# Optimization experiments

Measured on AMD Instinct MI355X. Metric: run time of the kernel, lower is better.

Reference implementation:

```python
import jax, jax.numpy as jnp
import numpy as np

B, N, M, K = 8, 9225, 4096, 32
D = 2          # coordinate dim
HID = 64       # MLP hidden
DOUT = 16      # MLP output / f_y channels


def setup_inputs() -> dict:
    key = jax.random.key(0)
    ks = jax.random.split(key, 10)
    y = jax.random.uniform(ks[0], (B, N, D), dtype=jnp.float32)
    x = jax.random.uniform(ks[1], (B, M, D), dtype=jnp.float32)
    f_y = jax.random.uniform(ks[2], (B, N, DOUT), dtype=jnp.float32)
    weights = jax.random.uniform(ks[3], (B, N), dtype=jnp.float32)
    neighbors_index = jax.random.randint(ks[4], (B, M, K), 0, N, dtype=jnp.int64)
    drop = jax.random.uniform(ks[5], (B, M, K)) < 0.1
    neighbors_index = jnp.where(drop, jnp.int64(-1), neighbors_index)
    # LinearChannelMLP params: 4 -> 64 -> 16, gelu between
    W1 = jax.random.normal(ks[6], (2 * D, HID), dtype=jnp.float32) * (1.0 / np.sqrt(2 * D))
    b1 = jnp.zeros((HID,), dtype=jnp.float32)
    W2 = jax.random.normal(ks[7], (HID, DOUT), dtype=jnp.float32) * (1.0 / np.sqrt(HID))
    b2 = jnp.zeros((DOUT,), dtype=jnp.float32)
    return {"y": y, "x": x, "f_y": f_y, "weights": weights,
            "W1": W1, "b1": b1, "W2": W2, "b2": b2,
            "neighbors_index": neighbors_index}


def _batched_gather(table, idx):
    # table: [B, N, ...], idx: [B, M, K] -> [B, M, K, ...]
    return jax.vmap(lambda t, i: t[i])(table, idx)


def reference(y, x, f_y, weights, W1, b1, W2, b2, neighbors_index):
    idx = jnp.where(neighbors_index == -1, 0, neighbors_index)      # [B,M,K]
    valid = (neighbors_index != -1).astype(y.dtype)[..., None]      # [B,M,K,1]

    rep_y = _batched_gather(y, idx)                                 # [B,M,K,D]
    in_f = _batched_gather(f_y, idx)                                # [B,M,K,DOUT]
    self_x = jnp.broadcast_to(x[:, :, None, :], rep_y.shape)        # [B,M,K,D]

    agg = jnp.concatenate([rep_y, self_x], axis=-1)                 # [B,M,K,2D]
    h = jax.nn.gelu(agg @ W1 + b1, approximate=False)               # [B,M,K,HID]
    kval = h @ W2 + b2                                              # [B,M,K,DOUT]

    kval = kval * in_f                                              # linear transform: k(x,y)*f(y)
    w_nbr = _batched_gather(weights, idx)[..., None]                # [B,M,K,1]
    kval = kval * w_nbr * valid
    return kval.sum(axis=2)                                         # [B,M,DOUT]
```

## Files before the change

### kernel.cpp

```cpp
#include <hip/hip_runtime.h>
#include <hip/hip_bf16.h>
#include <math.h>

#define B_    8
#define N_    9225
#define M_    4096
#define K_    32
#define HID_  64
#define DOUT_ 16
#define RPW   4

typedef __attribute__((ext_vector_type(8))) short short8;
typedef __attribute__((ext_vector_type(4))) float floatx4;
typedef __attribute__((ext_vector_type(2))) float f32x2;

static __device__ __forceinline__ short f2bf(float f) {
    __hip_bfloat16 h = __float2bfloat16(f);
    return __builtin_bit_cast(short, h);
}
static __device__ __forceinline__ f32x2 splat2(float v) { return (f32x2){v, v}; }

static __device__ __forceinline__ float row16_sum(float v) {
    int t;
    t = __builtin_amdgcn_update_dpp(0, __builtin_bit_cast(int, v), 0x111, 0xF, 0xF, true);
    v += __builtin_bit_cast(float, t);
    t = __builtin_amdgcn_update_dpp(0, __builtin_bit_cast(int, v), 0x112, 0xF, 0xF, true);
    v += __builtin_bit_cast(float, t);
    t = __builtin_amdgcn_update_dpp(0, __builtin_bit_cast(int, v), 0x114, 0xF, 0xF, true);
    v += __builtin_bit_cast(float, t);
    t = __builtin_amdgcn_update_dpp(0, __builtin_bit_cast(int, v), 0x118, 0xF, 0xF, true);
    v += __builtin_bit_cast(float, t);
    return v;
}

__global__ __launch_bounds__(256) void it_kernel(
    const float* __restrict__ y,
    const float* __restrict__ x,
    const float* __restrict__ f_y,
    const float* __restrict__ weights,
    const float* __restrict__ W1,
    const float* __restrict__ b1,
    const float* __restrict__ W2,
    const float* __restrict__ b2,
    const int*   __restrict__ nbr,
    float*       __restrict__ out)
{
    const int tid  = threadIdx.x;
    const int lane = tid & 63;
    const int q    = lane >> 4;
    const int nlo  = lane & 15;
    const int wave = blockIdx.x * 4 + (tid >> 6);

    f32x2 w1r[2][4][4];
    f32x2 b1r[2][4];
    #pragma unroll
    for (int ch = 0; ch < 2; ++ch) {
        #pragma unroll
        for (int i = 0; i < 4; ++i) {
            const floatx4 a0 = *(const floatx4*)(W1 + i*64 + ch*32 + q*8);
            const floatx4 a1 = *(const floatx4*)(W1 + i*64 + ch*32 + q*8 + 4);
            w1r[ch][i][0] = (f32x2){a0[0], a0[1]};
            w1r[ch][i][1] = (f32x2){a0[2], a0[3]};
            w1r[ch][i][2] = (f32x2){a1[0], a1[1]};
            w1r[ch][i][3] = (f32x2){a1[2], a1[3]};
        }
        const floatx4 c0 = *(const floatx4*)(b1 + ch*32 + q*8);
        const floatx4 c1 = *(const floatx4*)(b1 + ch*32 + q*8 + 4);
        b1r[ch][0] = (f32x2){c0[0], c0[1]};
        b1r[ch][1] = (f32x2){c0[2], c0[3]};
        b1r[ch][2] = (f32x2){c1[0], c1[1]};
        b1r[ch][3] = (f32x2){c1[2], c1[3]};
    }

    short8 w2f[2];
    #pragma unroll
    for (int ch = 0; ch < 2; ++ch)
        #pragma unroll
        for (int jj = 0; jj < 8; ++jj)
            w2f[ch][jj] = f2bf(W2[(ch*32 + q*8 + jj) * DOUT_ + nlo]);

    const floatx4 b2v = *(const floatx4*)(b2 + q*4);

    for (int it = 0; it < RPW; ++it) {
        const int row = wave * RPW + it;
        const int b   = row >> 12;
        const long bbase = (long)b * N_;
        const float2 xv = *(const float2*)(x + (size_t)row * 2);

        float  s[2]; float2 yv[2]; floatx4 fv[2];
        #pragma unroll
        for (int h = 0; h < 2; ++h) {
            const int  raw   = nbr[(size_t)row * K_ + h*16 + nlo];
            const bool valid = raw >= 0;
            const long bn    = bbase + (valid ? raw : 0);
            yv[h] = *(const float2*)(y + bn * 2);
            s[h]  = valid ? weights[bn] : 0.0f;
            fv[h] = *(const floatx4*)(f_y + bn * 16 + q*4);
        }

        float partial[4] = {0.f, 0.f, 0.f, 0.f};
        #pragma unroll
        for (int h = 0; h < 2; ++h) {
            short8 hf[2];
            #pragma unroll
            for (int ch = 0; ch < 2; ++ch) {
                #pragma unroll
                for (int p = 0; p < 4; ++p) {
                    f32x2 hin = b1r[ch][p];
                    hin = __builtin_elementwise_fma(splat2(yv[h].x), w1r[ch][0][p], hin);
                    hin = __builtin_elementwise_fma(splat2(yv[h].y), w1r[ch][1][p], hin);
                    hin = __builtin_elementwise_fma(splat2(xv.x),    w1r[ch][2][p], hin);
                    hin = __builtin_elementwise_fma(splat2(xv.y),    w1r[ch][3][p], hin);
                    const f32x2 hsq = hin * hin;
                    const f32x2 tt  = __builtin_elementwise_fma(hsq, splat2(0.07135481f),
                                                                splat2(1.59576912f));
                    const f32x2 z   = hin * tt;
                    const float e0  = __expf(z[0]);
                    const float e1  = __expf(z[1]);
                    const f32x2 r   = { __builtin_amdgcn_rcpf(1.0f + e0),
                                        __builtin_amdgcn_rcpf(1.0f + e1) };
                    const f32x2 g   = __builtin_elementwise_fma(-hin, r, hin);
                    hf[ch][2*p]     = f2bf(g[0]);
                    hf[ch][2*p + 1] = f2bf(g[1]);
                }
            }
            floatx4 acc = {0.f, 0.f, 0.f, 0.f};
            acc = __builtin_amdgcn_mfma_f32_16x16x32_bf16(w2f[0], hf[0], acc, 0, 0, 0);
            acc = __builtin_amdgcn_mfma_f32_16x16x32_bf16(w2f[1], hf[1], acc, 0, 0, 0);
            #pragma unroll
            for (int r4 = 0; r4 < 4; ++r4)
                partial[r4] = fmaf(acc[r4] + b2v[r4], fv[h][r4] * s[h], partial[r4]);
        }

        #pragma unroll
        for (int r4 = 0; r4 < 4; ++r4)
            partial[r4] = row16_sum(partial[r4]);

        if (nlo == 15) {
            floatx4 o = {partial[0], partial[1], partial[2], partial[3]};
            *(floatx4*)(out + (size_t)row * DOUT_ + q*4) = o;
        }
    }
}

extern "C" void kernel_launch(void* const* d_in, const int* in_sizes, int n_in,
                              void* d_out, int out_size, void* d_ws, size_t ws_size,
                              hipStream_t stream) {
    const float* y   = (const float*)d_in[0];
    const float* x   = (const float*)d_in[1];
    const float* f_y = (const float*)d_in[2];
    const float* w   = (const float*)d_in[3];
    const float* W1  = (const float*)d_in[4];
    const float* b1  = (const float*)d_in[5];
    const float* W2  = (const float*)d_in[6];
    const float* b2  = (const float*)d_in[7];
    const int*   nbr = (const int*)d_in[8];
    float* out = (float*)d_out;

    dim3 grid(B_ * M_ / (4 * RPW)), block(256);
    hipLaunchKernelGGL(it_kernel, grid, block, 0, stream,
                       y, x, f_y, w, W1, b1, W2, b2, nbr, out);
}
```

Baseline: 109.1 us.

## Prefetch neighbor gathers for all rows and replace exp-based GELU with rational tanh

Halves rows per wave and issues every row's gathers before any compute, so memory latency overlaps across rows and the grid has twice as many waves. It also swaps the exp plus reciprocal tanh-form GELU for a clamped Padé rational approximation of tanh that needs no exp. This holds more registers per wave, doubles weight-setup overhead per row, and adds approximation error on top of the existing tanh-vs-erf difference.

```diff
diff --git a/kernel.cpp b/kernel.cpp
--- a/kernel.cpp
+++ b/kernel.cpp
@@ -8,7 +8,7 @@
 #define K_    32
 #define HID_  64
 #define DOUT_ 16
-#define RPW   4
+#define RPW   2
 
 typedef __attribute__((ext_vector_type(8))) short short8;
 typedef __attribute__((ext_vector_type(4))) float floatx4;
@@ -33,6 +33,23 @@
     return v;
 }
 
+static __device__ __forceinline__ f32x2 gelu2(f32x2 x) {
+    const f32x2 xsq = x * x;
+    const f32x2 t   = __builtin_elementwise_fma(xsq, splat2(0.035677408f), splat2(0.79788456f));
+    const f32x2 z   = x * t;
+    const f32x2 u   = z * z;
+    const f32x2 a   = u + splat2(105.0f);
+    const f32x2 nin = __builtin_elementwise_fma(u, a, splat2(945.0f));
+    const f32x2 num = z * nin;
+    const f32x2 bq  = __builtin_elementwise_fma(u, splat2(15.0f), splat2(420.0f));
+    const f32x2 den = __builtin_elementwise_fma(u, bq, splat2(945.0f));
+    const f32x2 r   = { __builtin_amdgcn_rcpf(den[0]), __builtin_amdgcn_rcpf(den[1]) };
+    f32x2 th = num * r;
+    th = __builtin_elementwise_min(__builtin_elementwise_max(th, splat2(-1.0f)), splat2(1.0f));
+    const f32x2 hx = x * splat2(0.5f);
+    return __builtin_elementwise_fma(hx, th, hx);
+}
+
 __global__ __launch_bounds__(256) void it_kernel(
     const float* __restrict__ y,
     const float* __restrict__ x,
@@ -50,6 +67,7 @@
     const int q    = lane >> 4;
     const int nlo  = lane & 15;
     const int wave = blockIdx.x * 4 + (tid >> 6);
+    const int row0 = wave * RPW;
 
     f32x2 w1r[2][4][4];
     f32x2 b1r[2][4];
@@ -81,23 +99,27 @@
 
     const floatx4 b2v = *(const floatx4*)(b2 + q*4);
 
+    float  s[RPW][2]; float2 yv[RPW][2]; floatx4 fv[RPW][2]; float2 xv[RPW];
+    #pragma unroll
     for (int it = 0; it < RPW; ++it) {
-        const int row = wave * RPW + it;
+        const int row = row0 + it;
         const int b   = row >> 12;
         const long bbase = (long)b * N_;
-        const float2 xv = *(const float2*)(x + (size_t)row * 2);
-
-        float  s[2]; float2 yv[2]; floatx4 fv[2];
+        xv[it] = *(const float2*)(x + (size_t)row * 2);
         #pragma unroll
         for (int h = 0; h < 2; ++h) {
             const int  raw   = nbr[(size_t)row * K_ + h*16 + nlo];
             const bool valid = raw >= 0;
             const long bn    = bbase + (valid ? raw : 0);
-            yv[h] = *(const float2*)(y + bn * 2);
-            s[h]  = valid ? weights[bn] : 0.0f;
-            fv[h] = *(const floatx4*)(f_y + bn * 16 + q*4);
+            yv[it][h] = *(const float2*)(y + bn * 2);
+            s[it][h]  = valid ? weights[bn] : 0.0f;
+            fv[it][h] = *(const floatx4*)(f_y + bn * 16 + q*4);
         }
+    }
 
+    #pragma unroll
+    for (int it = 0; it < RPW; ++it) {
+        const int row = row0 + it;
         float partial[4] = {0.f, 0.f, 0.f, 0.f};
         #pragma unroll
         for (int h = 0; h < 2; ++h) {
@@ -107,19 +129,11 @@
                 #pragma unroll
                 for (int p = 0; p < 4; ++p) {
                     f32x2 hin = b1r[ch][p];
-                    hin = __builtin_elementwise_fma(splat2(yv[h].x), w1r[ch][0][p], hin);
-                    hin = __builtin_elementwise_fma(splat2(yv[h].y), w1r[ch][1][p], hin);
-                    hin = __builtin_elementwise_fma(splat2(xv.x),    w1r[ch][2][p], hin);
-                    hin = __builtin_elementwise_fma(splat2(xv.y),    w1r[ch][3][p], hin);
-                    const f32x2 hsq = hin * hin;
-                    const f32x2 tt  = __builtin_elementwise_fma(hsq, splat2(0.07135481f),
-                                                                splat2(1.59576912f));
-                    const f32x2 z   = hin * tt;
-                    const float e0  = __expf(z[0]);
-                    const float e1  = __expf(z[1]);
-                    const f32x2 r   = { __builtin_amdgcn_rcpf(1.0f + e0),
-                                        __builtin_amdgcn_rcpf(1.0f + e1) };
-                    const f32x2 g   = __builtin_elementwise_fma(-hin, r, hin);
+                    hin = __builtin_elementwise_fma(splat2(yv[it][h].x), w1r[ch][0][p], hin);
+                    hin = __builtin_elementwise_fma(splat2(yv[it][h].y), w1r[ch][1][p], hin);
+                    hin = __builtin_elementwise_fma(splat2(xv[it].x),    w1r[ch][2][p], hin);
+                    hin = __builtin_elementwise_fma(splat2(xv[it].y),    w1r[ch][3][p], hin);
+                    const f32x2 g = gelu2(hin);
                     hf[ch][2*p]     = f2bf(g[0]);
                     hf[ch][2*p + 1] = f2bf(g[1]);
                 }
@@ -129,7 +143,7 @@
             acc = __builtin_amdgcn_mfma_f32_16x16x32_bf16(w2f[1], hf[1], acc, 0, 0, 0);
             #pragma unroll
             for (int r4 = 0; r4 < 4; ++r4)
-                partial[r4] = fmaf(acc[r4] + b2v[r4], fv[h][r4] * s[h], partial[r4]);
+                partial[r4] = fmaf(acc[r4] + b2v[r4], fv[it][h][r4] * s[it][h], partial[r4]);
         }
 
         #pragma unroll
```

New measurement: 109.0 us. No clear change (-0.1%).
